# Performance work log

Measured on AMD Instinct MI355X. Metric: run time of the kernel, lower is better.

The kernel has to match this reference:

```python
import jax, jax.numpy as jnp
import numpy as np

H = 768
NH = 12
HD = H // NH
FF = 3072
E = 4
EPS = 1e-12


def _make_expert_params(key):
    ks = jax.random.split(key, 8)
    s = 0.02
    return {
        'wq': jax.random.normal(ks[0], (H, H), jnp.float32) * s,
        'wk': jax.random.normal(ks[1], (H, H), jnp.float32) * s,
        'wv': jax.random.normal(ks[2], (H, H), jnp.float32) * s,
        'wo': jax.random.normal(ks[3], (H, H), jnp.float32) * s,
        'bq': jnp.zeros((H,), jnp.float32),
        'bk': jnp.zeros((H,), jnp.float32),
        'bv': jnp.zeros((H,), jnp.float32),
        'bo': jnp.zeros((H,), jnp.float32),
        'ln1_g': jnp.ones((H,), jnp.float32),
        'ln1_b': jnp.zeros((H,), jnp.float32),
        'w1': jax.random.normal(ks[4], (H, FF), jnp.float32) * s,
        'b1': jnp.zeros((FF,), jnp.float32),
        'w2': jax.random.normal(ks[5], (FF, H), jnp.float32) * s,
        'b2': jnp.zeros((H,), jnp.float32),
        'ln2_g': jnp.ones((H,), jnp.float32),
        'ln2_b': jnp.zeros((H,), jnp.float32),
    }


def setup_inputs() -> dict:
    key = jax.random.key(0)
    k1, k2, kp = jax.random.split(key, 3)
    hidden_states = jax.random.normal(k1, (64, 128, H), jnp.float32)
    attention_mask = jnp.zeros((64, 128), jnp.float32)  # additive mask, 0 = attend
    centers = jax.random.normal(k2, (E, H), jnp.float32)
    pkeys = jax.random.split(kp, E)
    ps = [_make_expert_params(k) for k in pkeys]
    # stack expert params along leading axis for vectorized gather-by-expert
    params = {k: jnp.stack([p[k] for p in ps], axis=0) for k in ps[0]}
    out = {'hidden_states': hidden_states, 'attention_mask': attention_mask, 'centers': centers}
    out.update(params)
    return out


def _layernorm(x, g, b):
    mu = x.mean(-1, keepdims=True)
    var = ((x - mu) ** 2).mean(-1, keepdims=True)
    return (x - mu) * jax.lax.rsqrt(var + EPS) * g + b


def _encoder(x, mask, p):
    # x: [B,S,H], mask: [B,S] additive; p: per-sample expert params (leading dim B)
    B, S, _ = x.shape
    q = jnp.einsum('bsh,bhd->bsd', x, p['wq']) + p['bq'][:, None, :]
    k = jnp.einsum('bsh,bhd->bsd', x, p['wk']) + p['bk'][:, None, :]
    v = jnp.einsum('bsh,bhd->bsd', x, p['wv']) + p['bv'][:, None, :]
    q = q.reshape(B, S, NH, HD)
    k = k.reshape(B, S, NH, HD)
    v = v.reshape(B, S, NH, HD)
    scores = jnp.einsum('bqnd,bknd->bnqk', q, k) / np.sqrt(HD).astype(np.float32)
    scores = scores + mask[:, None, None, :]
    attn = jax.nn.softmax(scores, axis=-1)
    ctx = jnp.einsum('bnqk,bknd->bqnd', attn, v).reshape(B, S, H)
    att_out = jnp.einsum('bsh,bhd->bsd', ctx, p['wo']) + p['bo'][:, None, :]
    att_out = _layernorm(att_out + x, p['ln1_g'][:, None, :], p['ln1_b'][:, None, :])
    ffn = jnp.einsum('bsh,bhf->bsf', att_out, p['w1']) + p['b1'][:, None, :]
    ffn = jax.nn.gelu(ffn)
    ffn = jnp.einsum('bsf,bfh->bsh', ffn, p['w2']) + p['b2'][:, None, :]
    out = _layernorm(att_out + ffn, p['ln2_g'][:, None, :], p['ln2_b'][:, None, :])
    return out


def reference(hidden_states, attention_mask, centers,
              wq, wk, wv, wo, bq, bk, bv, bo, ln1_g, ln1_b,
              w1, b1, w2, b2, ln2_g, ln2_b):
    # routing: mean over seq, cdist to centers, argmin -> per-sentence expert id
    h_pca = hidden_states.mean(axis=1)  # [B,H]
    d2 = (jnp.sum(h_pca ** 2, -1, keepdims=True)
          - 2.0 * h_pca @ centers.T
          + jnp.sum(centers ** 2, -1)[None, :])
    eid = jnp.argmin(d2, axis=1)  # [B]
    params = {'wq': wq, 'wk': wk, 'wv': wv, 'wo': wo, 'bq': bq, 'bk': bk,
              'bv': bv, 'bo': bo, 'ln1_g': ln1_g, 'ln1_b': ln1_b,
              'w1': w1, 'b1': b1, 'w2': w2, 'b2': b2,
              'ln2_g': ln2_g, 'ln2_b': ln2_b}
    # gather per-sample expert params (jit-friendly, honors hard routing)
    psel = {k: v[eid] for k, v in params.items()}
    return _encoder(hidden_states, attention_mask, psel)
```

## Files before the change

kernel.cpp:

```cpp
#include <hip/hip_runtime.h>
#include <hip/hip_bf16.h>
#include <math.h>

#define HDIM 768
#define NHEAD 12
#define HEADD 64
#define FFDIM 3072
#define NEXP 4
#define SEQ 128
#define NB 64
#define QKVN 2304

typedef __attribute__((ext_vector_type(8))) _Float16 f16x8;
typedef __attribute__((ext_vector_type(4))) _Float16 f16x4;
typedef __attribute__((ext_vector_type(4))) float f32x4;

__device__ __forceinline__ float gelu_fast(float x) {
  float t = -1.5957691216057308f * x * __builtin_fmaf(0.044715f * x, x, 1.0f);
  return x * __builtin_amdgcn_rcpf(1.0f + __expf(t));
}

__device__ __forceinline__ void gld_lds16(const void* g, void* l) {
  __builtin_amdgcn_global_load_lds(
      (const __attribute__((address_space(1))) unsigned int*)g,
      (__attribute__((address_space(3))) unsigned int*)l, 16, 0, 0);
}

__global__ __launch_bounds__(256) void route_cvt_kernel(
    const float* __restrict__ hs, const float* __restrict__ centers,
    int* __restrict__ eid, _Float16* __restrict__ x16) {
  int b = blockIdx.x, t = threadIdx.x;
  __shared__ float hp[HDIM];
  __shared__ float dist[NEXP];
  const float* xb = hs + (size_t)b * SEQ * HDIM;
  _Float16* ob = x16 + (size_t)b * SEQ * HDIM;

  if (t < 192) {
    float p0 = 0.f, p1 = 0.f, p2 = 0.f, p3 = 0.f;
    for (int sq = 0; sq < SEQ; ++sq) {
      float4 v = ((const float4*)(xb + (size_t)sq * HDIM))[t];
      p0 += v.x; p1 += v.y; p2 += v.z; p3 += v.w;
      f16x4 h = {(_Float16)v.x, (_Float16)v.y, (_Float16)v.z, (_Float16)v.w};
      *(f16x4*)(ob + (size_t)sq * HDIM + t * 4) = h;
    }
    hp[t * 4 + 0] = p0 * (1.0f / SEQ);
    hp[t * 4 + 1] = p1 * (1.0f / SEQ);
    hp[t * 4 + 2] = p2 * (1.0f / SEQ);
    hp[t * 4 + 3] = p3 * (1.0f / SEQ);
  }
  if (t < NEXP) dist[t] = 0.f;
  __syncthreads();

  float pe[NEXP] = {0.f, 0.f, 0.f, 0.f};
  for (int h = t; h < HDIM; h += 256) {
    float v = hp[h];
#pragma unroll
    for (int e = 0; e < NEXP; ++e) {
      float d = v - centers[e * HDIM + h];
      pe[e] += d * d;
    }
  }
#pragma unroll
  for (int e = 0; e < NEXP; ++e) atomicAdd(&dist[e], pe[e]);
  __syncthreads();
  if (t == 0) {
    int best = 0; float bv = dist[0];
    for (int e = 1; e < NEXP; ++e) if (dist[e] < bv) { bv = dist[e]; best = e; }
    eid[b] = best;
  }
}

__device__ __forceinline__ void tr_tile(const float* __restrict__ ip,
                                        _Float16* __restrict__ op,
                                        int K, int N, int nb, int kb,
                                        float (*tile)[33], int t) {
  int tx = t & 31, ty = t >> 5;
  for (int i = ty; i < 32; i += 8)
    tile[i][tx] = ip[(size_t)(kb + i) * N + nb + tx];
  __syncthreads();
  for (int i = ty; i < 32; i += 8)
    op[(size_t)(nb + i) * K + kb + tx] = (_Float16)tile[tx][i];
}

__global__ __launch_bounds__(256) void prep_weights(
    const float* __restrict__ wq, const float* __restrict__ wk,
    const float* __restrict__ wv, const float* __restrict__ wo,
    const float* __restrict__ w1, const float* __restrict__ w2,
    const float* __restrict__ bq, const float* __restrict__ bk,
    const float* __restrict__ bv,
    _Float16* __restrict__ Wqkvt, _Float16* __restrict__ Wot,
    _Float16* __restrict__ W1t, _Float16* __restrict__ W2t,
    float* __restrict__ bqkv, const int* __restrict__ eid,
    int* __restrict__ order, int* __restrict__ ord_eid) {
  __shared__ float tile[32][33];
  int x = blockIdx.x, e = blockIdx.y, t = threadIdx.x;

  if (x < 1728) {
    int which = x / 576, local = x % 576;
    const float* src = (which == 0) ? wq : (which == 1) ? wk : wv;
    tr_tile(src + (size_t)e * HDIM * HDIM,
            Wqkvt + (size_t)which * HDIM * HDIM + (size_t)e * QKVN * HDIM,
            HDIM, HDIM, (local % 24) * 32, (local / 24) * 32, tile, t);
  } else if (x < 2304) {
    int local = x - 1728;
    tr_tile(wo + (size_t)e * HDIM * HDIM, Wot + (size_t)e * HDIM * HDIM,
            HDIM, HDIM, (local % 24) * 32, (local / 24) * 32, tile, t);
  } else if (x < 4608) {
    int local = x - 2304;
    tr_tile(w1 + (size_t)e * HDIM * FFDIM, W1t + (size_t)e * FFDIM * HDIM,
            HDIM, FFDIM, (local % 96) * 32, (local / 96) * 32, tile, t);
  } else if (x < 6912) {
    int local = x - 4608;
    tr_tile(w2 + (size_t)e * FFDIM * HDIM, W2t + (size_t)e * HDIM * FFDIM,
            FFDIM, HDIM, (local % 24) * 32, (local / 24) * 32, tile, t);
  } else if (x < 6948) {
    if (e == 0) {
      int i = (x - 6912) * 256 + t;
      if (i < NEXP * QKVN) {
        int ee = i / QKVN, n = i % QKVN;
        float v = (n < HDIM) ? bq[ee * HDIM + n]
                : (n < 2 * HDIM) ? bk[ee * HDIM + n - HDIM]
                                 : bv[ee * HDIM + n - 2 * HDIM];
        bqkv[i] = v;
      }
    }
  } else {
    if (e == 0 && t == 0) {
      int n = 0;
      for (int ee = 0; ee < NEXP; ++ee)
        for (int b = 0; b < NB; ++b)
          if (eid[b] == ee) { order[n] = b; ord_eid[n] = ee; n++; }
    }
  }
}

template <int OUT_F16, int GELU, int KDIM, int SPLITK>
__global__ __launch_bounds__(256) void gemm_mfma(
    const _Float16* __restrict__ A, const _Float16* __restrict__ Wt,
    const float* __restrict__ Ball, const int* __restrict__ order,
    const int* __restrict__ ord_eid, void* __restrict__ Cv, int N) {
  constexpr int K = KDIM;
  constexpr int Kp = KDIM / SPLITK;
  int GX = N >> 7;
  int L = blockIdx.x;
  int low3 = L & 7, Mq = L >> 3;
  int x = Mq % GX, zhi = Mq / GX;
  int z = zhi * 8 + low3;
  int b = order[z];
  int e = ord_eid[z];
  int col0 = x * 128;
  int kz = blockIdx.y;
  int kbeg = kz * Kp;

  int t = threadIdx.x;
  int lane = t & 63, w = t >> 6;
  int quad = lane >> 4, l16 = lane & 15;
  int wr = (w >> 1) * 64, wc = (w & 1) * 64;

  __shared__ __align__(16) _Float16 As[128 * 32];
  __shared__ __align__(16) _Float16 Bs[128 * 32];

  const _Float16* Ab = A + (size_t)b * SEQ * K + kbeg;
  const _Float16* Wb = Wt + (size_t)e * N * K + (size_t)col0 * K + kbeg;

  int e0 = t * 8, e1 = 2048 + t * 8;
  int m0 = e0 >> 5, k0e = e0 & 31;
  int m1 = e1 >> 5, k1e = e1 & 31;
  const _Float16* ga0 = Ab + (size_t)m0 * K + k0e;
  const _Float16* ga1 = Ab + (size_t)m1 * K + k1e;
  const _Float16* gb0 = Wb + (size_t)m0 * K + k0e;
  const _Float16* gb1 = Wb + (size_t)m1 * K + k1e;
  _Float16* lA0 = &As[e0]; _Float16* lA1 = &As[e1];
  _Float16* lB0 = &Bs[e0]; _Float16* lB1 = &Bs[e1];

  f32x4 acc[4][4];
#pragma unroll
  for (int i = 0; i < 4; ++i)
#pragma unroll
    for (int j = 0; j < 4; ++j) acc[i][j] = (f32x4){0.f, 0.f, 0.f, 0.f};

#pragma unroll
  for (int kk = 0; kk < Kp; kk += 32) {
    gld_lds16(ga0 + kk, lA0);
    gld_lds16(ga1 + kk, lA1);
    gld_lds16(gb0 + kk, lB0);
    gld_lds16(gb1 + kk, lB1);
    __syncthreads();
    f16x8 af[4], bf[4];
#pragma unroll
    for (int i = 0; i < 4; ++i)
      af[i] = *(const f16x8*)&As[(wr + i * 16 + l16) * 32 + quad * 8];
#pragma unroll
    for (int i = 0; i < 4; ++i)
      bf[i] = *(const f16x8*)&Bs[(wc + i * 16 + l16) * 32 + quad * 8];
#pragma unroll
    for (int i = 0; i < 4; ++i)
#pragma unroll
      for (int j = 0; j < 4; ++j)
        acc[i][j] = __builtin_amdgcn_mfma_f32_16x16x32_f16(af[i], bf[j], acc[i][j], 0, 0, 0);
    __syncthreads();
  }

  const float* bias = Ball + (size_t)e * N;

  if (OUT_F16) {
    _Float16* Ch = (_Float16*)Cv + (size_t)b * SEQ * N;
#pragma unroll
    for (int i = 0; i < 4; ++i)
#pragma unroll
      for (int j = 0; j < 4; ++j) {
        int col = col0 + wc + j * 16 + l16;
        float bv = bias[col];
#pragma unroll
        for (int r = 0; r < 4; ++r) {
          int row = wr + i * 16 + quad * 4 + r;
          float v = acc[i][j][r] + bv;
          if (GELU) v = gelu_fast(v);
          Ch[(size_t)row * N + col] = (_Float16)v;
        }
      }
  } else {
    float* Cf = (float*)Cv + (size_t)kz * NB * SEQ * N + (size_t)b * SEQ * N;
    float bscale = (kz == 0) ? 1.f : 0.f;
#pragma unroll
    for (int i = 0; i < 4; ++i)
#pragma unroll
      for (int j = 0; j < 4; ++j) {
        int col = col0 + wc + j * 16 + l16;
        float bv = bias[col] * bscale;
#pragma unroll
        for (int r = 0; r < 4; ++r) {
          int row = wr + i * 16 + quad * 4 + r;
          Cf[(size_t)row * N + col] = acc[i][j][r] + bv;
        }
      }
  }
}

__global__ __launch_bounds__(256) void attn_mfma(
    const _Float16* __restrict__ QKV, const float* __restrict__ mask,
    _Float16* __restrict__ Ctx) {
  int h = blockIdx.x, b = blockIdx.y;
  int t = threadIdx.x;
  int w = t >> 6, lane = t & 63, quad = lane >> 4, l16 = lane & 15;

  __shared__ __align__(16) char smem[54784];
  _Float16* Qs = (_Float16*)smem;
  _Float16* Ks = (_Float16*)(smem + 18432);
  _Float16* Ps = (_Float16*)smem;
  _Float16* Vt = (_Float16*)(smem + 36864);
  float* mrow = (float*)(smem + 54272);

  const _Float16* Qb = QKV + (size_t)b * SEQ * QKVN + h * HEADD;
  const _Float16* Kb = Qb + HDIM;
  const _Float16* Vb = Qb + 2 * HDIM;

#pragma unroll
  for (int it = 0; it < 4; ++it) {
    int chunk = t + it * 256;
    int row = chunk >> 3, c = chunk & 7;
    *(f16x8*)&Qs[row * 72 + c * 8] = *(const f16x8*)(Qb + (size_t)row * QKVN + c * 8);
    *(f16x8*)&Ks[row * 72 + c * 8] = *(const f16x8*)(Kb + (size_t)row * QKVN + c * 8);
  }
  {
    int vc = t & 7, vjp0 = t >> 3;
#pragma unroll
    for (int it = 0; it < 2; ++it) {
      int jp = vjp0 + it * 32;
      f16x8 v0 = *(const f16x8*)(Vb + (size_t)(2 * jp) * QKVN + vc * 8);
      f16x8 v1 = *(const f16x8*)(Vb + (size_t)(2 * jp + 1) * QKVN + vc * 8);
#pragma unroll
      for (int i = 0; i < 8; ++i) {
        int d = vc * 8 + i;
        unsigned ua = __builtin_bit_cast(unsigned short, (_Float16)v0[i]);
        unsigned ub = __builtin_bit_cast(unsigned short, (_Float16)v1[i]);
        ((unsigned*)Vt)[d * 68 + jp] = ua | (ub << 16);
      }
    }
  }
  if (t < SEQ) mrow[t] = mask[(size_t)b * SEQ + t];
  __syncthreads();

  int m0 = w * 32;
  f32x4 accs[2][8];
#pragma unroll
  for (int i = 0; i < 2; ++i)
#pragma unroll
    for (int j = 0; j < 8; ++j) accs[i][j] = (f32x4){0.f, 0.f, 0.f, 0.f};

#pragma unroll
  for (int ks = 0; ks < 2; ++ks) {
    int k0 = ks * 32 + quad * 8;
    f16x8 af[2], bf[8];
#pragma unroll
    for (int i = 0; i < 2; ++i)
      af[i] = *(const f16x8*)&Qs[(m0 + i * 16 + l16) * 72 + k0];
#pragma unroll
    for (int j = 0; j < 8; ++j)
      bf[j] = *(const f16x8*)&Ks[(j * 16 + l16) * 72 + k0];
#pragma unroll
    for (int i = 0; i < 2; ++i)
#pragma unroll
      for (int j = 0; j < 8; ++j)
        accs[i][j] = __builtin_amdgcn_mfma_f32_16x16x32_f16(af[i], bf[j], accs[i][j], 0, 0, 0);
  }
  __syncthreads();

  float mv[8];
#pragma unroll
  for (int j = 0; j < 8; ++j) mv[j] = mrow[j * 16 + l16];

  float linv[2][4];
#pragma unroll
  for (int i = 0; i < 2; ++i) {
#pragma unroll
    for (int j = 0; j < 8; ++j)
#pragma unroll
      for (int r = 0; r < 4; ++r)
        accs[i][j][r] = accs[i][j][r] * 0.125f + mv[j];
#pragma unroll
    for (int r = 0; r < 4; ++r) {
      float m = accs[i][0][r];
#pragma unroll
      for (int j = 1; j < 8; ++j) m = fmaxf(m, accs[i][j][r]);
      m = fmaxf(m, __shfl_xor(m, 1));
      m = fmaxf(m, __shfl_xor(m, 2));
      m = fmaxf(m, __shfl_xor(m, 4));
      m = fmaxf(m, __shfl_xor(m, 8));
      float sum = 0.f;
#pragma unroll
      for (int j = 0; j < 8; ++j) {
        float p = __expf(accs[i][j][r] - m);
        accs[i][j][r] = p;
        sum += p;
      }
      sum += __shfl_xor(sum, 1);
      sum += __shfl_xor(sum, 2);
      sum += __shfl_xor(sum, 4);
      sum += __shfl_xor(sum, 8);
      linv[i][r] = 1.f / sum;
    }
    int rowb = m0 + i * 16 + quad * 4;
#pragma unroll
    for (int j = 0; j < 8; ++j)
#pragma unroll
      for (int r = 0; r < 4; ++r)
        Ps[(rowb + r) * 136 + j * 16 + l16] = (_Float16)accs[i][j][r];
  }
  __syncthreads();

  f32x4 acco[2][4];
#pragma unroll
  for (int i = 0; i < 2; ++i)
#pragma unroll
    for (int j = 0; j < 4; ++j) acco[i][j] = (f32x4){0.f, 0.f, 0.f, 0.f};

#pragma unroll
  for (int ks = 0; ks < 4; ++ks) {
    int k0 = ks * 32 + quad * 8;
    f16x8 pa[2], vf[4];
#pragma unroll
    for (int i = 0; i < 2; ++i)
      pa[i] = *(const f16x8*)&Ps[(m0 + i * 16 + l16) * 136 + k0];
#pragma unroll
    for (int j = 0; j < 4; ++j)
      vf[j] = *(const f16x8*)&Vt[(j * 16 + l16) * 136 + k0];
#pragma unroll
    for (int i = 0; i < 2; ++i)
#pragma unroll
      for (int j = 0; j < 4; ++j)
        acco[i][j] = __builtin_amdgcn_mfma_f32_16x16x32_f16(pa[i], vf[j], acco[i][j], 0, 0, 0);
  }

  _Float16* Cb = Ctx + (size_t)b * SEQ * HDIM + h * HEADD;
#pragma unroll
  for (int i = 0; i < 2; ++i)
#pragma unroll
    for (int j = 0; j < 4; ++j)
#pragma unroll
      for (int r = 0; r < 4; ++r) {
        int row = m0 + i * 16 + quad * 4 + r;
        int d = j * 16 + l16;
        Cb[(size_t)row * HDIM + d] = (_Float16)(acco[i][j][r] * linv[i][r]);
      }
}

template <int NP>
__global__ __launch_bounds__(256) void resid_ln_kernel(
    const float* __restrict__ X, const float* __restrict__ P0,
    const float* __restrict__ P1,
    const float* __restrict__ Gall, const float* __restrict__ Ball,
    const int* __restrict__ eid, float* __restrict__ Out,
    _Float16* __restrict__ Out16) {
  int row = blockIdx.x, b = blockIdx.y, t = threadIdx.x;
  int e = eid[b];
  size_t off = ((size_t)b * SEQ + row) * HDIM;
  const float* x = X + off;
  const float* p0 = P0 + off;
  const float* p1 = (NP > 1) ? P1 + off : nullptr;
  float* o = Out + off;
  const float* g = Gall + (size_t)e * HDIM;
  const float* bb = Ball + (size_t)e * HDIM;

  __shared__ float buf[HDIM];
  __shared__ float red[256];

  float s = 0.f;
  for (int h = t; h < HDIM; h += 256) {
    float v = x[h] + p0[h];
    if (NP > 1) v += p1[h];
    buf[h] = v;
    s += v;
  }
  red[t] = s;
  __syncthreads();
  for (int off2 = 128; off2 > 0; off2 >>= 1) {
    if (t < off2) red[t] += red[t + off2];
    __syncthreads();
  }
  float mean = red[0] * (1.0f / HDIM);
  __syncthreads();

  float s2 = 0.f;
  for (int h = t; h < HDIM; h += 256) {
    float d = buf[h] - mean;
    s2 += d * d;
  }
  red[t] = s2;
  __syncthreads();
  for (int off2 = 128; off2 > 0; off2 >>= 1) {
    if (t < off2) red[t] += red[t + off2];
    __syncthreads();
  }
  float var = red[0] * (1.0f / HDIM);
  float rs = rsqrtf(var + 1e-12f);

  for (int h = t; h < HDIM; h += 256) {
    float v = (buf[h] - mean) * rs * g[h] + bb[h];
    o[h] = v;
    if (Out16) Out16[off + h] = (_Float16)v;
  }
}

extern "C" void kernel_launch(void* const* d_in, const int* in_sizes, int n_in,
                              void* d_out, int out_size, void* d_ws, size_t ws_size,
                              hipStream_t stream) {
  const float* hs   = (const float*)d_in[0];
  const float* mask = (const float*)d_in[1];
  const float* cen  = (const float*)d_in[2];
  const float* wq = (const float*)d_in[3];
  const float* wk = (const float*)d_in[4];
  const float* wv = (const float*)d_in[5];
  const float* wo = (const float*)d_in[6];
  const float* bq = (const float*)d_in[7];
  const float* bk = (const float*)d_in[8];
  const float* bv = (const float*)d_in[9];
  const float* bo = (const float*)d_in[10];
  const float* ln1g = (const float*)d_in[11];
  const float* ln1b = (const float*)d_in[12];
  const float* w1 = (const float*)d_in[13];
  const float* b1 = (const float*)d_in[14];
  const float* w2 = (const float*)d_in[15];
  const float* b2 = (const float*)d_in[16];
  const float* ln2g = (const float*)d_in[17];
  const float* ln2b = (const float*)d_in[18];
  float* out = (float*)d_out;

  const size_t sh = (size_t)SEQ * HDIM;

  char* p = (char*)d_ws;
  int* eid = (int*)p;                 p += 256;
  int* order = (int*)p;               p += 256;
  int* ord_eid = (int*)p;             p += 256;
  float* bqkv = (float*)p;            p += (size_t)NEXP * QKVN * 4;
  _Float16* Wqkvt = (_Float16*)p;     p += (size_t)NEXP * QKVN * HDIM * 2;
  _Float16* Wot = (_Float16*)p;       p += (size_t)NEXP * HDIM * HDIM * 2;
  _Float16* W1t = (_Float16*)p;       p += (size_t)NEXP * FFDIM * HDIM * 2;
  _Float16* W2t = (_Float16*)p;       p += (size_t)NEXP * HDIM * FFDIM * 2;
  _Float16* x16 = (_Float16*)p;       p += (size_t)NB * sh * 2;

  char* region = p;                   p += (size_t)NB * SEQ * QKVN * 2;
  _Float16* ctx16 = (_Float16*)p;     p += (size_t)NB * sh * 2;
  float* aof = (float*)p;             p += (size_t)NB * sh * 4;
  _Float16* ao16 = (_Float16*)p;      p += (size_t)NB * sh * 2;
  char* ffreg = p;                    p += (size_t)NB * SEQ * FFDIM * 2;

  float* woparts = (float*)ffreg;
  float* w2parts = (float*)region;
  _Float16* ff16 = (_Float16*)ffreg;

  route_cvt_kernel<<<NB, 256, 0, stream>>>(hs, cen, eid, x16);
  prep_weights<<<dim3(6949, NEXP), 256, 0, stream>>>(
      wq, wk, wv, wo, w1, w2, bq, bk, bv,
      Wqkvt, Wot, W1t, W2t, bqkv, eid, order, ord_eid);
  gemm_mfma<1, 0, HDIM, 1><<<dim3((QKVN / 128) * NB, 1), 256, 0, stream>>>(
      x16, Wqkvt, bqkv, order, ord_eid, region, QKVN);
  attn_mfma<<<dim3(NHEAD, NB), 256, 0, stream>>>(
      (const _Float16*)region, mask, ctx16);
  gemm_mfma<0, 0, HDIM, 2><<<dim3((HDIM / 128) * NB, 2), 256, 0, stream>>>(
      ctx16, Wot, bo, order, ord_eid, woparts, HDIM);
  resid_ln_kernel<2><<<dim3(SEQ, NB), 256, 0, stream>>>(
      hs, woparts, woparts + (size_t)NB * sh, ln1g, ln1b, eid, aof, ao16);
  gemm_mfma<1, 1, HDIM, 1><<<dim3((FFDIM / 128) * NB, 1), 256, 0, stream>>>(
      ao16, W1t, b1, order, ord_eid, ff16, FFDIM);
  gemm_mfma<0, 0, FFDIM, 2><<<dim3((HDIM / 128) * NB, 2), 256, 0, stream>>>(
      ff16, W2t, b2, order, ord_eid, w2parts, HDIM);
  resid_ln_kernel<2><<<dim3(SEQ, NB), 256, 0, stream>>>(
      aof, w2parts, w2parts + (size_t)NB * sh, ln2g, ln2b, eid, out,
      (_Float16*)nullptr);
}
```

Before: 473.3 us.

## Triple-buffer LDS tiles in MFMA GEMM with async prefetch two stages ahead

```diff
diff --git a/kernel.cpp b/kernel.cpp
--- a/kernel.cpp
+++ b/kernel.cpp
@@ -141,6 +141,7 @@
     const int* __restrict__ ord_eid, void* __restrict__ Cv, int N) {
   constexpr int K = KDIM;
   constexpr int Kp = KDIM / SPLITK;
+  constexpr int NIT = Kp / 32;
   int GX = N >> 7;
   int L = blockIdx.x;
   int low3 = L & 7, Mq = L >> 3;
@@ -157,8 +158,8 @@
   int quad = lane >> 4, l16 = lane & 15;
   int wr = (w >> 1) * 64, wc = (w & 1) * 64;
 
-  __shared__ __align__(16) _Float16 As[128 * 32];
-  __shared__ __align__(16) _Float16 Bs[128 * 32];
+  __shared__ __align__(16) _Float16 As[3 * 128 * 32];
+  __shared__ __align__(16) _Float16 Bs[3 * 128 * 32];
 
   const _Float16* Ab = A + (size_t)b * SEQ * K + kbeg;
   const _Float16* Wb = Wt + (size_t)e * N * K + (size_t)col0 * K + kbeg;
@@ -170,8 +171,16 @@
   const _Float16* ga1 = Ab + (size_t)m1 * K + k1e;
   const _Float16* gb0 = Wb + (size_t)m0 * K + k0e;
   const _Float16* gb1 = Wb + (size_t)m1 * K + k1e;
-  _Float16* lA0 = &As[e0]; _Float16* lA1 = &As[e1];
-  _Float16* lB0 = &Bs[e0]; _Float16* lB1 = &Bs[e1];
+
+  auto issue = [&](int c, int st) {
+    int off = c * 32;
+    _Float16* Ast = As + st * 4096;
+    _Float16* Bst = Bs + st * 4096;
+    gld_lds16(ga0 + off, Ast + e0);
+    gld_lds16(ga1 + off, Ast + e1);
+    gld_lds16(gb0 + off, Bst + e0);
+    gld_lds16(gb1 + off, Bst + e1);
+  };
 
   f32x4 acc[4][4];
 #pragma unroll
@@ -179,26 +188,32 @@
 #pragma unroll
     for (int j = 0; j < 4; ++j) acc[i][j] = (f32x4){0.f, 0.f, 0.f, 0.f};
 
-#pragma unroll
-  for (int kk = 0; kk < Kp; kk += 32) {
-    gld_lds16(ga0 + kk, lA0);
-    gld_lds16(ga1 + kk, lA1);
-    gld_lds16(gb0 + kk, lB0);
-    gld_lds16(gb1 + kk, lB1);
-    __syncthreads();
+  issue(0, 0);
+  if (NIT > 1) issue(1, 1);
+
+#pragma unroll
+  for (int it = 0; it < NIT; ++it) {
+    if (it < NIT - 1) __builtin_amdgcn_s_waitcnt(0xF74);
+    else              __builtin_amdgcn_s_waitcnt(0xF70);
+    __builtin_amdgcn_s_barrier();
+
+    int st = it % 3;
+    const _Float16* Ast = As + st * 4096;
+    const _Float16* Bst = Bs + st * 4096;
     f16x8 af[4], bf[4];
 #pragma unroll
     for (int i = 0; i < 4; ++i)
-      af[i] = *(const f16x8*)&As[(wr + i * 16 + l16) * 32 + quad * 8];
+      af[i] = *(const f16x8*)&Ast[(wr + i * 16 + l16) * 32 + quad * 8];
 #pragma unroll
     for (int i = 0; i < 4; ++i)
-      bf[i] = *(const f16x8*)&Bs[(wc + i * 16 + l16) * 32 + quad * 8];
+      bf[i] = *(const f16x8*)&Bst[(wc + i * 16 + l16) * 32 + quad * 8];
 #pragma unroll
     for (int i = 0; i < 4; ++i)
 #pragma unroll
       for (int j = 0; j < 4; ++j)
         acc[i][j] = __builtin_amdgcn_mfma_f32_16x16x32_f16(af[i], bf[j], acc[i][j], 0, 0, 0);
-    __syncthreads();
+
+    if (it + 2 < NIT) issue(it + 2, (it + 2) % 3);
   }
 
   const float* bias = Ball + (size_t)e * N;
```

Result: no change. 467.5 us (-1.2%).
